# Optimization experiments

Hardware: AMD Instinct MI355X
Metric: run time of the kernel (lower is better)

Reference implementation:

```python
import jax, jax.numpy as jnp
import numpy as np

MASK_FUTURE = True


def setup_inputs() -> dict:
    key = jax.random.key(0)
    kq, kk, kv = jax.random.split(key, 3)
    B, S, D = 4, 4096, 64
    query = jax.random.normal(kq, (B, S, D), dtype=jnp.float32)
    k = jax.random.normal(kk, (B, S, D), dtype=jnp.float32)
    value = jax.random.normal(kv, (B, S, D), dtype=jnp.float32)
    attention_mask = jnp.ones((B, S), dtype=jnp.int32)
    return {"query": query, "key": k, "value": value, "attention_mask": attention_mask}


def reference(query, key, value, attention_mask):
    B, Sq, D = query.shape
    Sk = key.shape[1]
    scale = 1.0 / jnp.sqrt(jnp.asarray(D, dtype=query.dtype))
    # [B, Sq, Sk] masked scaled scores
    scores = jnp.einsum("bqd,bkd->bqk", query, key) * scale
    valid = attention_mask[:, None, :] != 0  # padding mask, [B,1,Sk]
    if MASK_FUTURE and Sq == Sk:
        causal = jnp.arange(Sk)[None, :] <= jnp.arange(Sq)[:, None]  # [Sq,Sk]
        valid = valid & causal[None, :, :]
    scores = jnp.where(valid, scores, -jnp.inf)
    weights = jax.nn.softmax(scores, axis=-1)
    return jnp.einsum("bqk,bkd->bqd", weights, value)
```

## Files before the change

kernel.cpp:

```cpp
#include <hip/hip_runtime.h>
#include <hip/hip_bf16.h>

#define S_LEN 4096
#define DHEAD 64
#define KBLK 64
#define CSZ 8
#define NS 8
#define FM 12.0f

typedef __attribute__((ext_vector_type(8))) short bf16x8;
typedef __attribute__((ext_vector_type(8))) unsigned short u16x8;
typedef __attribute__((ext_vector_type(4))) float f32x4;

__device__ __forceinline__ unsigned short f2bf(float f) {
    union { float f; unsigned u; } v; v.f = f;
    unsigned r = v.u + 0x7fffu + ((v.u >> 16) & 1u);
    return (unsigned short)(r >> 16);
}

__device__ __forceinline__ float bf2f(unsigned short h) {
    union { unsigned u; float f; } v; v.u = ((unsigned)h) << 16; return v.f;
}

__device__ __forceinline__ unsigned pack_bf2(float a, float b) {
    __hip_bfloat162 h = __float22bfloat162_rn(float2{a, b});
    union { __hip_bfloat162 h; unsigned u; } cv; cv.h = h;
    return cv.u;
}

__device__ __forceinline__ float exp2_raw(float x) {
    float r;
    asm volatile("v_exp_f32 %0, %1\n\ts_nop 0" : "=v"(r) : "v"(x));
    return r;
}

__device__ __forceinline__ void gl_lds16(const void* g, void* l) {
    __builtin_amdgcn_global_load_lds(
        (const __attribute__((address_space(1))) void*)g,
        (__attribute__((address_space(3))) void*)l, 16, 0, 0);
}

__global__ __launch_bounds__(256) void prep(
        const float* __restrict__ K, const float* __restrict__ V,
        unsigned short* __restrict__ Kb, unsigned short* __restrict__ Vb)
{
    __shared__ float Vlds[64 * 65];

    const int tile = blockIdx.x;
    const int b = tile >> 6, kt = tile & 63;
    const float* kp = K + ((size_t)(b * S_LEN + kt * KBLK)) * DHEAD;
    const float* vp = V + ((size_t)(b * S_LEN + kt * KBLK)) * DHEAD;
    unsigned short* kb = Kb + (size_t)tile * 4096;
    unsigned short* vb = Vb + (size_t)tile * 4096;
    const int tid = threadIdx.x;

    #pragma unroll
    for (int r = 0; r < 4; ++r) {
        int idx = (r * 256 + tid) * 4;
        int k = idx >> 6, d = idx & 63;
        float4 v = *(const float4*)(vp + idx);
        Vlds[k * 65 + d]     = v.x;
        Vlds[k * 65 + d + 1] = v.y;
        Vlds[k * 65 + d + 2] = v.z;
        Vlds[k * 65 + d + 3] = v.w;
    }
    __syncthreads();

    #pragma unroll
    for (int r = 0; r < 2; ++r) {
        int ci = r * 256 + tid;
        int base = ci * 16;
        int kr = base >> 7;
        int low = (base & 127) ^ ((kr & 7) << 4);
        int d0 = low >> 1;
        u16x8 o;
        #pragma unroll
        for (int j = 0; j < 8; ++j) o[j] = f2bf(kp[kr * DHEAD + d0 + j]);
        *(u16x8*)(kb + ci * 8) = o;
    }
    #pragma unroll
    for (int r = 0; r < 2; ++r) {
        int ci = r * 256 + tid;
        int base = ci * 16;
        int d = base >> 7;
        int low = (base & 127) ^ (((d >> 1) & 7) << 4);
        int slot0 = low >> 1;
        u16x8 o;
        #pragma unroll
        for (int j = 0; j < 8; ++j) {
            int slot = slot0 + j;
            int ct = 2 * ((slot >> 2) & 1) + ((slot >> 5) & 1);
            int k = ct * 16 + ((slot >> 3) & 3) * 4 + (slot & 3);
            o[j] = f2bf(Vlds[k * 65 + d]);
        }
        *(u16x8*)(vb + ci * 8) = o;
    }
}

__global__ __launch_bounds__(256) void attn_part(
        const float* __restrict__ Q, const unsigned short* __restrict__ Kb,
        const unsigned short* __restrict__ Vb, const int* __restrict__ mask,
        unsigned short* __restrict__ O_part, float* __restrict__ l_part, int Bn)
{
    __shared__ __align__(16) unsigned short K_lds[2][4096];
    __shared__ __align__(16) unsigned short V_lds[2][4096];
    __shared__ __align__(16) float mb[2][KBLK];

    const int blk = blockIdx.x;
    const int c   = blk & (NS - 1);
    const int bq  = 63 - ((blk >> 3) & 63);
    const int b   = blk >> 9;
    const int nt  = bq + 1;
    const int k0  = c * CSZ;
    if (k0 >= nt) return;
    const int k1  = (k0 + CSZ < nt) ? (k0 + CSZ) : nt;

    const int tid = threadIdx.x;
    const int lane = tid & 63;
    const int wq = tid >> 6;
    const int l15 = lane & 15;
    const int l4 = lane >> 4;
    const int q0 = bq * 64;
    const int qg = q0 + wq * 16 + l15;

    const float sc = 0.125f * 1.44269504088896340736f;

    bf16x8 qf[2];
    {
        const float* qp = Q + ((size_t)(b * S_LEN + qg)) * DHEAD + l4 * 8;
        for (int kk = 0; kk < 2; ++kk) {
            float4 a = *(const float4*)(qp + kk * 32);
            float4 cq = *(const float4*)(qp + kk * 32 + 4);
            bf16x8 f;
            f[0] = (short)f2bf(a.x * sc); f[1] = (short)f2bf(a.y * sc);
            f[2] = (short)f2bf(a.z * sc); f[3] = (short)f2bf(a.w * sc);
            f[4] = (short)f2bf(cq.x * sc); f[5] = (short)f2bf(cq.y * sc);
            f[6] = (short)f2bf(cq.z * sc); f[7] = (short)f2bf(cq.w * sc);
            qf[kk] = f;
        }
    }

    int mreg;
    auto STAGE = [&](int kt, int buf) {
        const unsigned short* kb = Kb + ((size_t)(b * 64 + kt)) * 4096;
        const unsigned short* vb = Vb + ((size_t)(b * 64 + kt)) * 4096;
        #pragma unroll
        for (int r = 0; r < 2; ++r) {
            int ci = r * 256 + tid;
            int ub = (r * 256 + wq * 64) * 16;
            gl_lds16(kb + ci * 8, (char*)&K_lds[buf][0] + ub);
            gl_lds16(vb + ci * 8, (char*)&V_lds[buf][0] + ub);
        }
        mreg = mask[(size_t)b * S_LEN + kt * KBLK + lane];
    };

    f32x4 acc[4];
    for (int t = 0; t < 4; ++t) acc[t] = (f32x4){0.f, 0.f, 0.f, 0.f};
    f32x4 lacc = (f32x4){0.f, 0.f, 0.f, 0.f};

    STAGE(k0, 0);
    if (tid < KBLK) mb[0][tid] = mreg ? -FM : -INFINITY;
    __syncthreads();
    int cur = 0;

    for (int kt = k0; kt < k1; ++kt) {
        const bool more = (kt + 1 < k1);
        if (more) STAGE(kt + 1, cur ^ 1);

        f32x4 s[4];
        __builtin_amdgcn_s_setprio(1);
        #pragma unroll
        for (int ct = 0; ct < 4; ++ct) {
            f32x4 z = (f32x4){0.f, 0.f, 0.f, 0.f};
            #pragma unroll
            for (int kk = 0; kk < 2; ++kk) {
                int row = ct * 16 + l15;
                int byte = (row * 128 + (l4 * 8 + kk * 32) * 2) ^ ((row & 7) << 4);
                bf16x8 kf = *(const bf16x8*)((const char*)&K_lds[cur][0] + byte);
                z = __builtin_amdgcn_mfma_f32_16x16x32_bf16(kf, qf[kk], z, 0, 0, 0);
            }
            s[ct] = z;
        }
        __builtin_amdgcn_s_setprio(0);

        const bool diag = (kt == nt - 1);
        f32x4 p[4];
        #pragma unroll
        for (int ct = 0; ct < 4; ++ct) {
            f32x4 bias4 = *(const f32x4*)&mb[cur][ct * 16 + l4 * 4];
            f32x4 v = s[ct] + bias4;
            if (diag) {
                int kb_ = kt * 64 + ct * 16 + l4 * 4;
                #pragma unroll
                for (int i = 0; i < 4; ++i)
                    if (kb_ + i > qg) v[i] = -INFINITY;
            }
            f32x4 pe;
            pe[0] = exp2_raw(v[0]); pe[1] = exp2_raw(v[1]);
            pe[2] = exp2_raw(v[2]); pe[3] = exp2_raw(v[3]);
            p[ct] = pe;
            lacc += pe;
        }

        bf16x8 pf[2];
        #pragma unroll
        for (int kk = 0; kk < 2; ++kk) {
            union { unsigned u[4]; bf16x8 v; } pk;
            pk.u[0] = pack_bf2(p[kk][0], p[kk][1]);
            pk.u[1] = pack_bf2(p[kk][2], p[kk][3]);
            pk.u[2] = pack_bf2(p[kk + 2][0], p[kk + 2][1]);
            pk.u[3] = pack_bf2(p[kk + 2][2], p[kk + 2][3]);
            pf[kk] = pk.v;
        }

        __builtin_amdgcn_s_setprio(1);
        #pragma unroll
        for (int kk = 0; kk < 2; ++kk) {
            #pragma unroll
            for (int t = 0; t < 4; ++t) {
                int d = t * 16 + l15;
                int vbyte = (d * 128 + (l4 * 8 + kk * 32) * 2) ^ (((d >> 1) & 7) << 4);
                bf16x8 vf = *(const bf16x8*)((const char*)&V_lds[cur][0] + vbyte);
                acc[t] = __builtin_amdgcn_mfma_f32_16x16x32_bf16(pf[kk], vf, acc[t], 0, 0, 0);
            }
        }
        __builtin_amdgcn_s_setprio(0);

        if (more && tid < KBLK) mb[cur ^ 1][tid] = mreg ? -FM : -INFINITY;
        __syncthreads();
        cur ^= 1;
    }

    float la = lacc[0] + lacc[1] + lacc[2] + lacc[3];
    la += __shfl_xor(la, 16);
    la += __shfl_xor(la, 32);

    for (int i = 0; i < 4; ++i) {
        int qr = q0 + wq * 16 + l4 * 4 + i;
        size_t rb = ((size_t)c * Bn + b) * S_LEN + qr;
        unsigned short* op = O_part + rb * 64 + l15;
        #pragma unroll
        for (int t = 0; t < 4; ++t)
            op[t * 16] = f2bf(acc[t][i]);
    }
    if (l4 == 0) {
        size_t rb = ((size_t)c * Bn + b) * S_LEN + qg;
        l_part[rb] = la;
    }
}

__global__ __launch_bounds__(256) void attn_reduce(
        const unsigned short* __restrict__ O_part, const float* __restrict__ l_part,
        float* __restrict__ out, int Bn)
{
    int g = blockIdx.x * 256 + threadIdx.x;
    int row = g >> 4;
    int qd  = (g & 15) * 4;
    int b = row >> 12;
    int q = row & (S_LEN - 1);
    int nc = (q >> 9) + 1;

    float den = 0.f;
    f32x4 acc = (f32x4){0.f, 0.f, 0.f, 0.f};
    for (int cc = 0; cc < nc; ++cc) {
        size_t rb = ((size_t)cc * Bn + b) * S_LEN + q;
        den += l_part[rb];
        uint2 u = *(const uint2*)(O_part + rb * 64 + qd);
        acc[0] += bf2f((unsigned short)(u.x & 0xffff));
        acc[1] += bf2f((unsigned short)(u.x >> 16));
        acc[2] += bf2f((unsigned short)(u.y & 0xffff));
        acc[3] += bf2f((unsigned short)(u.y >> 16));
    }
    float inv = 1.0f / den;
    float4 o;
    o.x = acc[0] * inv; o.y = acc[1] * inv;
    o.z = acc[2] * inv; o.w = acc[3] * inv;
    *(float4*)(out + ((size_t)b * S_LEN + q) * 64 + qd) = o;
}

__global__ __launch_bounds__(256) void attn_fwd(
        const float* __restrict__ Q, const float* __restrict__ K,
        const float* __restrict__ V, const int* __restrict__ mask,
        float* __restrict__ out)
{
    __shared__ __align__(16) unsigned short K_lds[KBLK * DHEAD];
    __shared__ __align__(16) unsigned short Vt_lds[DHEAD * KBLK];
    __shared__ __align__(16) unsigned short P_lds[4 * 16 * KBLK];
    __shared__ float mb[KBLK];

    const int tid = threadIdx.x;
    const int lane = tid & 63;
    const int wq = tid >> 6;
    const int l15 = lane & 15;
    const int l4 = lane >> 4;

    const int bq = blockIdx.x & 63;
    const int b  = blockIdx.x >> 6;
    const int q0 = bq * 64;
    const int nt = bq + 1;

    const float sc = 0.125f * 1.44269504088896340736f;

    bf16x8 qf[2];
    {
        const float* qp = Q + ((size_t)(b * S_LEN + q0 + wq * 16 + l15)) * DHEAD + l4 * 8;
        for (int kk = 0; kk < 2; ++kk) {
            float4 a = *(const float4*)(qp + kk * 32);
            float4 c = *(const float4*)(qp + kk * 32 + 4);
            bf16x8 f;
            f[0] = (short)f2bf(a.x * sc); f[1] = (short)f2bf(a.y * sc);
            f[2] = (short)f2bf(a.z * sc); f[3] = (short)f2bf(a.w * sc);
            f[4] = (short)f2bf(c.x * sc); f[5] = (short)f2bf(c.y * sc);
            f[6] = (short)f2bf(c.z * sc); f[7] = (short)f2bf(c.w * sc);
            qf[kk] = f;
        }
    }

    float4 kv[4];
    float4 vv[4];
    int    mreg;
    const int rp_  = (tid >> 4) << 1;
    const int d4v_ = (tid & 15) << 2;

    auto LOAD_TILE = [&](int kt) {
        const float* kp = K + ((size_t)(b * S_LEN + kt * KBLK)) * DHEAD;
        #pragma unroll
        for (int r = 0; r < 4; ++r) {
            int qi = tid + 256 * r;
            int kr = qi >> 4, d4 = (qi & 15) << 2;
            kv[r] = *(const float4*)(kp + kr * DHEAD + d4);
        }
        const float* vp = V + ((size_t)(b * S_LEN + kt * KBLK)) * DHEAD;
        #pragma unroll
        for (int r = 0; r < 2; ++r) {
            int row0 = rp_ + r * 32;
            vv[2 * r]     = *(const float4*)(vp + row0 * DHEAD + d4v_);
            vv[2 * r + 1] = *(const float4*)(vp + (row0 + 1) * DHEAD + d4v_);
        }
        mreg = mask[(size_t)b * S_LEN + kt * KBLK + (tid & 63)];
    };

    auto WRITE_TILE = [&]() {
        #pragma unroll
        for (int r = 0; r < 4; ++r) {
            int qi = tid + 256 * r;
            int kr = qi >> 4, d4 = (qi & 15) << 2;
            float4 v = kv[r];
            uint2 h;
            h.x = pack_bf2(v.x, v.y);
            h.y = pack_bf2(v.z, v.w);
            int byte = (kr * 128 + d4 * 2) ^ ((kr & 7) << 4);
            *(uint2*)((char*)K_lds + byte) = h;
        }
        #pragma unroll
        for (int r = 0; r < 2; ++r) {
            int row0 = rp_ + r * 32;
            float4 a = vv[2 * r];
            float4 c = vv[2 * r + 1];
            #pragma unroll
            for (int j = 0; j < 4; ++j) {
                int d = d4v_ + j;
                float aj = (j == 0) ? a.x : (j == 1) ? a.y : (j == 2) ? a.z : a.w;
                float cj = (j == 0) ? c.x : (j == 1) ? c.y : (j == 2) ? c.z : c.w;
                unsigned pack = pack_bf2(aj, cj);
                int byte = (d * 128 + row0 * 2) ^ ((d & 7) << 4);
                *(unsigned*)((char*)Vt_lds + byte) = pack;
            }
        }
        if (tid < KBLK)
            mb[tid] = mreg ? -FM : -INFINITY;
    };

    f32x4 acc[4];
    for (int t = 0; t < 4; ++t) acc[t] = (f32x4){0.f, 0.f, 0.f, 0.f};
    float l_acc[4] = {0.f, 0.f, 0.f, 0.f};

    LOAD_TILE(0);

    for (int kt = 0; kt < nt; ++kt) {
        __syncthreads();
        WRITE_TILE();
        __syncthreads();
        if (kt + 1 < nt) LOAD_TILE(kt + 1);

        f32x4 s[4];
        for (int ct = 0; ct < 4; ++ct) {
            f32x4 z = (f32x4){0.f, 0.f, 0.f, 0.f};
            for (int kk = 0; kk < 2; ++kk) {
                int row = ct * 16 + l15;
                int byte = (row * 128 + (l4 * 8 + kk * 32) * 2) ^ ((row & 7) << 4);
                bf16x8 kf = *(const bf16x8*)((const char*)K_lds + byte);
                z = __builtin_amdgcn_mfma_f32_16x16x32_bf16(qf[kk], kf, z, 0, 0, 0);
            }
            s[ct] = z;
        }

        const bool diag = (kt == nt - 1);
        for (int ct = 0; ct < 4; ++ct) {
            float bias = mb[ct * 16 + l15];
            int colg = kt * KBLK + ct * 16 + l15;
            for (int i = 0; i < 4; ++i) {
                float v = s[ct][i] + bias;
                if (diag) {
                    int qg2 = q0 + wq * 16 + l4 * 4 + i;
                    if (colg > qg2) v = -INFINITY;
                }
                float p = exp2_raw(v);
                l_acc[i] += p;
                int row = l4 * 4 + i;
                int col = ct * 16 + l15;
                int byte = (row * 128 + col * 2) ^ ((row & 7) << 4);
                *(unsigned short*)((char*)P_lds + wq * 2048 + byte) = f2bf(p);
            }
        }

        for (int kk = 0; kk < 2; ++kk) {
            int pbyte = (l15 * 128 + (l4 * 8 + kk * 32) * 2) ^ ((l15 & 7) << 4);
            bf16x8 pf = *(const bf16x8*)((const char*)P_lds + wq * 2048 + pbyte);
            for (int t = 0; t < 4; ++t) {
                int d = t * 16 + l15;
                int vbyte = (d * 128 + (l4 * 8 + kk * 32) * 2) ^ ((d & 7) << 4);
                bf16x8 vf = *(const bf16x8*)((const char*)Vt_lds + vbyte);
                acc[t] = __builtin_amdgcn_mfma_f32_16x16x32_bf16(pf, vf, acc[t], 0, 0, 0);
            }
        }
    }

    for (int i = 0; i < 4; ++i) {
        float v = l_acc[i];
        v += __shfl_xor(v, 1);
        v += __shfl_xor(v, 2);
        v += __shfl_xor(v, 4);
        v += __shfl_xor(v, 8);
        l_acc[i] = v;
    }

    for (int i = 0; i < 4; ++i) {
        float inv = 1.0f / l_acc[i];
        int qg2 = q0 + wq * 16 + l4 * 4 + i;
        float* op = out + ((size_t)(b * S_LEN + qg2)) * DHEAD + l15;
        for (int t = 0; t < 4; ++t)
            op[t * 16] = acc[t][i] * inv;
    }
}

extern "C" void kernel_launch(void* const* d_in, const int* in_sizes, int n_in,
                              void* d_out, int out_size, void* d_ws, size_t ws_size,
                              hipStream_t stream) {
    const float* Q = (const float*)d_in[0];
    const float* K = (const float*)d_in[1];
    const float* V = (const float*)d_in[2];
    const int* mask = (const int*)d_in[3];
    float* out = (float*)d_out;
    int Bn = in_sizes[0] / (S_LEN * DHEAD);

    size_t oN = (size_t)NS * Bn * S_LEN * 64;
    size_t lN = (size_t)NS * Bn * S_LEN;
    size_t bN = (size_t)Bn * 64 * 4096;
    size_t need = oN * 2 + lN * 4 + bN * 2 * 2;
    if (ws_size >= need) {
        unsigned short* O_part = (unsigned short*)d_ws;
        float* l_part = (float*)(O_part + oN);
        unsigned short* Kb = (unsigned short*)(l_part + lN);
        unsigned short* Vb = Kb + bN;
        prep<<<dim3(Bn * 64), dim3(256), 0, stream>>>(K, V, Kb, Vb);
        attn_part<<<dim3(Bn * 64 * NS), dim3(256), 0, stream>>>(
            Q, Kb, Vb, mask, O_part, l_part, Bn);
        attn_reduce<<<dim3(Bn * S_LEN * 16 / 256), dim3(256), 0, stream>>>(
            O_part, l_part, out, Bn);
    } else {
        attn_fwd<<<dim3(Bn * 64), dim3(256), 0, stream>>>(Q, K, V, mask, out);
    }
}
```

Baseline: 48.28 us.

## Triple-buffer K/V tiles and precompute mask bias in prep kernel

Raises the LDS staging pipeline in the attention partial kernel from double to triple buffering, prefetching two tiles ahead with explicit vmcnt waits and raw s_barrier in place of __syncthreads. The per-tile mask-to-bias conversion moves into the prep kernel, which writes a float bias array to workspace; the main loop then reads the bias straight from global memory instead of staging it through shared memory. The aim is to hide global-load latency and cut per-iteration synchronization, at the cost of more LDS per block (which may lower occupancy) and a global bias load inside the loop.

```diff
diff --git a/kernel.cpp b/kernel.cpp
--- a/kernel.cpp
+++ b/kernel.cpp
@@ -42,7 +42,9 @@
 
 __global__ __launch_bounds__(256) void prep(
         const float* __restrict__ K, const float* __restrict__ V,
-        unsigned short* __restrict__ Kb, unsigned short* __restrict__ Vb)
+        const int* __restrict__ mask,
+        unsigned short* __restrict__ Kb, unsigned short* __restrict__ Vb,
+        float* __restrict__ Mb)
 {
     __shared__ float Vlds[64 * 65];
 
@@ -95,16 +97,18 @@
         }
         *(u16x8*)(vb + ci * 8) = o;
     }
+    if (tid < KBLK)
+        Mb[(size_t)tile * 64 + tid] =
+            mask[(size_t)b * S_LEN + kt * KBLK + tid] ? -FM : -INFINITY;
 }
 
 __global__ __launch_bounds__(256) void attn_part(
         const float* __restrict__ Q, const unsigned short* __restrict__ Kb,
-        const unsigned short* __restrict__ Vb, const int* __restrict__ mask,
+        const unsigned short* __restrict__ Vb, const float* __restrict__ Mb,
         unsigned short* __restrict__ O_part, float* __restrict__ l_part, int Bn)
 {
-    __shared__ __align__(16) unsigned short K_lds[2][4096];
-    __shared__ __align__(16) unsigned short V_lds[2][4096];
-    __shared__ __align__(16) float mb[2][KBLK];
+    __shared__ __align__(16) unsigned short K_lds[3][4096];
+    __shared__ __align__(16) unsigned short V_lds[3][4096];
 
     const int blk = blockIdx.x;
     const int c   = blk & (NS - 1);
@@ -140,7 +144,6 @@
         }
     }
 
-    int mreg;
     auto STAGE = [&](int kt, int buf) {
         const unsigned short* kb = Kb + ((size_t)(b * 64 + kt)) * 4096;
         const unsigned short* vb = Vb + ((size_t)(b * 64 + kt)) * 4096;
@@ -151,7 +154,6 @@
             gl_lds16(kb + ci * 8, (char*)&K_lds[buf][0] + ub);
             gl_lds16(vb + ci * 8, (char*)&V_lds[buf][0] + ub);
         }
-        mreg = mask[(size_t)b * S_LEN + kt * KBLK + lane];
     };
 
     f32x4 acc[4];
@@ -159,13 +161,26 @@
     f32x4 lacc = (f32x4){0.f, 0.f, 0.f, 0.f};
 
     STAGE(k0, 0);
-    if (tid < KBLK) mb[0][tid] = mreg ? -FM : -INFINITY;
-    __syncthreads();
-    int cur = 0;
-
+    const bool two = (k0 + 1 < k1);
+    if (two) {
+        STAGE(k0 + 1, 1);
+        asm volatile("s_waitcnt vmcnt(4)" ::: "memory");
+    } else {
+        asm volatile("s_waitcnt vmcnt(0)" ::: "memory");
+    }
+    __builtin_amdgcn_sched_barrier(0);
+    __builtin_amdgcn_s_barrier();
+    __builtin_amdgcn_sched_barrier(0);
+
+    int sl = 0;
     for (int kt = k0; kt < k1; ++kt) {
-        const bool more = (kt + 1 < k1);
-        if (more) STAGE(kt + 1, cur ^ 1);
+        const bool haveN2 = (kt + 2 < k1);
+        if (haveN2) {
+            int st = sl + 2; if (st >= 3) st -= 3;
+            STAGE(kt + 2, st);
+        }
+
+        const float* mbp = Mb + ((size_t)(b * 64 + kt)) * 64;
 
         f32x4 s[4];
         __builtin_amdgcn_s_setprio(1);
@@ -176,7 +191,7 @@
             for (int kk = 0; kk < 2; ++kk) {
                 int row = ct * 16 + l15;
                 int byte = (row * 128 + (l4 * 8 + kk * 32) * 2) ^ ((row & 7) << 4);
-                bf16x8 kf = *(const bf16x8*)((const char*)&K_lds[cur][0] + byte);
+                bf16x8 kf = *(const bf16x8*)((const char*)&K_lds[sl][0] + byte);
                 z = __builtin_amdgcn_mfma_f32_16x16x32_bf16(kf, qf[kk], z, 0, 0, 0);
             }
             s[ct] = z;
@@ -187,7 +202,7 @@
         f32x4 p[4];
         #pragma unroll
         for (int ct = 0; ct < 4; ++ct) {
-            f32x4 bias4 = *(const f32x4*)&mb[cur][ct * 16 + l4 * 4];
+            f32x4 bias4 = *(const f32x4*)(mbp + ct * 16 + l4 * 4);
             f32x4 v = s[ct] + bias4;
             if (diag) {
                 int kb_ = kt * 64 + ct * 16 + l4 * 4;
@@ -220,15 +235,20 @@
             for (int t = 0; t < 4; ++t) {
                 int d = t * 16 + l15;
                 int vbyte = (d * 128 + (l4 * 8 + kk * 32) * 2) ^ (((d >> 1) & 7) << 4);
-                bf16x8 vf = *(const bf16x8*)((const char*)&V_lds[cur][0] + vbyte);
+                bf16x8 vf = *(const bf16x8*)((const char*)&V_lds[sl][0] + vbyte);
                 acc[t] = __builtin_amdgcn_mfma_f32_16x16x32_bf16(pf[kk], vf, acc[t], 0, 0, 0);
             }
         }
         __builtin_amdgcn_s_setprio(0);
 
-        if (more && tid < KBLK) mb[cur ^ 1][tid] = mreg ? -FM : -INFINITY;
-        __syncthreads();
-        cur ^= 1;
+        if (kt + 1 < k1) {
+            if (haveN2) asm volatile("s_waitcnt vmcnt(4)" ::: "memory");
+            else        asm volatile("s_waitcnt vmcnt(0)" ::: "memory");
+            __builtin_amdgcn_sched_barrier(0);
+            __builtin_amdgcn_s_barrier();
+            __builtin_amdgcn_sched_barrier(0);
+        }
+        sl = (sl == 2) ? 0 : sl + 1;
     }
 
     float la = lacc[0] + lacc[1] + lacc[2] + lacc[3];
@@ -457,15 +477,17 @@
     size_t oN = (size_t)NS * Bn * S_LEN * 64;
     size_t lN = (size_t)NS * Bn * S_LEN;
     size_t bN = (size_t)Bn * 64 * 4096;
-    size_t need = oN * 2 + lN * 4 + bN * 2 * 2;
+    size_t mN = (size_t)Bn * 64 * 64;
+    size_t need = oN * 2 + lN * 4 + bN * 2 * 2 + mN * 4;
     if (ws_size >= need) {
         unsigned short* O_part = (unsigned short*)d_ws;
         float* l_part = (float*)(O_part + oN);
         unsigned short* Kb = (unsigned short*)(l_part + lN);
         unsigned short* Vb = Kb + bN;
-        prep<<<dim3(Bn * 64), dim3(256), 0, stream>>>(K, V, Kb, Vb);
+        float* Mb = (float*)(Vb + bN);
+        prep<<<dim3(Bn * 64), dim3(256), 0, stream>>>(K, V, mask, Kb, Vb, Mb);
         attn_part<<<dim3(Bn * 64 * NS), dim3(256), 0, stream>>>(
-            Q, Kb, Vb, mask, O_part, l_part, Bn);
+            Q, Kb, Vb, Mb, O_part, l_part, Bn);
         attn_reduce<<<dim3(Bn * S_LEN * 16 / 256), dim3(256), 0, stream>>>(
             O_part, l_part, out, Bn);
     } else {
```

Result: slower. 58.04 us (+20.2%).
